# Performance work log

Hardware: AMD Instinct MI355X
Metric: run time of the kernel (lower is better)

The kernel has to match this reference:

```python
import jax, jax.numpy as jnp
import numpy as np


def setup_inputs() -> dict:
    key = jax.random.key(0)
    k1, k2, k3, k4, k5 = jax.random.split(key, 5)
    B, C, H, W = 4, 256, 64, 64
    INTER = 128
    # NOTE: original inits out.weight to zeros (residual identity at init);
    # we use small random weights so the reference exercises the full math.
    s = 0.02
    return {
        "x": jax.random.normal(k1, (B, C, H, W), dtype=jnp.float32),
        "w_theta": jax.random.normal(k2, (INTER, C), dtype=jnp.float32) * s,
        "w_phi": jax.random.normal(k3, (INTER, C), dtype=jnp.float32) * s,
        "w_g": jax.random.normal(k4, (INTER, C), dtype=jnp.float32) * s,
        "w_out": jax.random.normal(k5, (C, INTER), dtype=jnp.float32) * s,
    }


def reference(x, w_theta, w_phi, w_g, w_out):
    B, C, H, W = x.shape
    N = H * W
    xf = x.reshape(B, C, N)                      # [B, C, N]
    theta = jnp.einsum("ic,bcn->bni", w_theta, xf)  # [B, N, inter]
    phi = jnp.einsum("ic,bcn->bin", w_phi, xf)      # [B, inter, N]
    g = jnp.einsum("ic,bcn->bni", w_g, xf)          # [B, N, inter]
    attn = jax.nn.softmax(jnp.einsum("bni,bim->bnm", theta, phi), axis=-1)  # [B, N, N]
    y = jnp.einsum("bnm,bmi->bin", attn, g)         # [B, inter, N]
    out = jnp.einsum("ci,bin->bcn", w_out, y)       # [B, C, N]
    return x + out.reshape(B, C, H, W)
```

## Files before the change

kernel.cpp:

```cpp
#include <hip/hip_runtime.h>
#include <hip/hip_bf16.h>
#include <cstdint>

#define BATCH 4
#define CDIM 256
#define NTOK 4096
#define IDIM 128
#define NSP 8

typedef __attribute__((ext_vector_type(4))) float f32x4;
typedef __attribute__((ext_vector_type(16))) float f32x16;
typedef __attribute__((ext_vector_type(8))) short short8;

static __device__ __forceinline__ unsigned cvt_pk(float lo, float hi) {
  unsigned r;
  asm("v_cvt_pk_bf16_f32 %0, %1, %2" : "=v"(r) : "v"(lo), "v"(hi));
  return r;
}
static __device__ __forceinline__ float bf2f(unsigned short u) {
  union { unsigned u; float f; } v;
  v.u = (unsigned)u << 16;
  return v.f;
}
static __device__ __forceinline__ float exp2_f(float x) {
#if __has_builtin(__builtin_amdgcn_exp2f)
  return __builtin_amdgcn_exp2f(x);
#else
  return exp2f(x);
#endif
}
static __device__ __forceinline__ unsigned pk_fp8x4(float a, float b, float c, float d) {
  unsigned r = 0;
#if __has_builtin(__builtin_amdgcn_cvt_pk_fp8_f32)
  r = __builtin_amdgcn_cvt_pk_fp8_f32(a, b, r, false);
  r = __builtin_amdgcn_cvt_pk_fp8_f32(c, d, r, true);
#else
  asm("v_cvt_pk_fp8_f32 %0, %1, %2" : "+v"(r) : "v"(a), "v"(b));
  asm("v_cvt_pk_fp8_f32 %0, %1, %2 op_sel:[0,0,1]" : "+v"(r) : "v"(c), "v"(d));
#endif
  return r;
}

__global__ __launch_bounds__(256) void cast_w_kernel(
    const float* __restrict__ wt, const float* __restrict__ wp,
    const float* __restrict__ wg, const float* __restrict__ wo,
    unsigned short* __restrict__ Wb)
{
  int id = blockIdx.x * 256 + threadIdx.x;
  if (id < 24576) {
    int pidx = id >> 13;
    int rem = id & 8191;
    int i = rem >> 6, c4 = (rem & 63) * 4;
    const float* src = pidx == 0 ? wt : pidx == 1 ? wp : wg;
    float4 v = *(const float4*)&src[i * 256 + c4];
    float s = (pidx == 0) ? 1.4426950408889634f : 1.0f;
    uint2 u = make_uint2(cvt_pk(v.x * s, v.y * s), cvt_pk(v.z * s, v.w * s));
    *(uint2*)&Wb[(((size_t)pidx * 32 + (c4 >> 3)) * 128 + i) * 8 + (c4 & 7)] = u;
  } else {
    int rem = id - 24576;
    int c = rem >> 5, i4 = (rem & 31) * 4;
    float4 v = *(const float4*)&wo[c * 128 + i4];
    uint2 u = make_uint2(cvt_pk(v.x, v.y), cvt_pk(v.z, v.w));
    *(uint2*)&Wb[98304 + (((size_t)(i4 >> 3) * 256 + c) * 8) + (i4 & 7)] = u;
  }
}

__global__ __launch_bounds__(768) void qkv_kernel(
    const float* __restrict__ x, const unsigned short* __restrict__ Wb,
    unsigned char* __restrict__ Qf, unsigned char* __restrict__ Kf,
    unsigned short* __restrict__ Vf)
{
  __shared__ __align__(16) unsigned short xt[64 * 256];
  __shared__ __align__(16) unsigned short sc[8][16 * 128];

  const int b = blockIdx.y;
  const int n0 = blockIdx.x * 64;
  const int t = threadIdx.x;
  const float* xb = x + (size_t)b * CDIM * NTOK;

  for (int it = 0; it < 3; ++it) {
    int u = it * 768 + t;
    if (u < 2048) {
      int c0 = (u >> 4) * 2;
      int n4 = (u & 15) * 4;
      float4 va = *(const float4*)&xb[(size_t)c0 * NTOK + n0 + n4];
      float4 vb = *(const float4*)&xb[(size_t)(c0 + 1) * NTOK + n0 + n4];
      const float* pa = (const float*)&va;
      const float* pb = (const float*)&vb;
#pragma unroll
      for (int j = 0; j < 4; ++j) {
        int n = n4 + j;
        unsigned pk = cvt_pk(pa[j], pb[j]);
        *(unsigned*)((char*)xt + n * 512 + ((c0 * 2) ^ ((n & 15) << 4))) = pk;
      }
    }
  }
  __syncthreads();

  const int lane = t & 63;
  const int wv = __builtin_amdgcn_readfirstlane(t >> 6);
  const int nsub = wv & 3, proj = wv >> 2;
  const int cl = lane & 15, g = lane >> 4;

  f32x4 acc[8];
#pragma unroll
  for (int i = 0; i < 8; ++i) acc[i] = (f32x4){0.f, 0.f, 0.f, 0.f};

  const int nrow = nsub * 16 + cl;
  const int swz = (nrow & 15) << 4;
#pragma unroll
  for (int kc = 0; kc < 8; ++kc) {
    int cb = kc * 32 + g * 8;
    short8 af = *(const short8*)((const char*)xt + nrow * 512 + ((cb * 2) ^ swz));
#pragma unroll
    for (int is = 0; is < 8; ++is) {
      short8 bf = *(const short8*)&Wb[(((size_t)proj * 32 + kc * 4 + g) * 128 +
                                       is * 16 + cl) * 8];
      acc[is] = __builtin_amdgcn_mfma_f32_16x16x32_bf16(af, bf, acc[is], 0, 0, 0);
    }
  }

  if (proj < 2) {
    unsigned short* scw = sc[wv];
#pragma unroll
    for (int is = 0; is < 8; ++is)
#pragma unroll
      for (int r = 0; r < 4; ++r) {
        int nl = g * 4 + r;
        int i2 = (is * 16 + cl) * 2;
        *(unsigned short*)((char*)scw + nl * 256 + (i2 ^ ((nl & 15) << 4))) =
            (unsigned short)cvt_pk(acc[is][r], 0.f);
      }
    unsigned char* dstF = (proj == 0 ? Qf : Kf) + (size_t)b * (NTOK * IDIM);
    const int r = lane & 15;
    const int n = n0 + nsub * 16 + r;
    const size_t ntbase = (size_t)(n >> 5) * 4096;
#pragma unroll
    for (int u = 0; u < 4; ++u) {
      int c = (lane >> 4) + 4 * u;
      short8 v8 = *(const short8*)((const char*)scw + r * 256 +
                                   ((c * 16) ^ ((r & 15) << 4)));
      float f[8];
#pragma unroll
      for (int e = 0; e < 8; ++e) f[e] = bf2f((unsigned short)v8[e]);
      uint2 w = make_uint2(pk_fp8x4(f[0], f[1], f[2], f[3]),
                           pk_fp8x4(f[4], f[5], f[6], f[7]));
      size_t off = ntbase + (size_t)(c >> 1) * 512 +
                   (size_t)((n & 31) + 32 * (c & 1)) * 8;
      *(uint2*)(dstF + off) = w;
    }
  } else {
    unsigned short* dstV = Vf + (size_t)b * (IDIM * NTOK) +
                           (size_t)((n0 >> 4) + nsub) * 2048;
#pragma unroll
    for (int is = 0; is < 8; ++is) {
      int itv = is >> 1;
      int l2 = (is & 1) * 16 + cl + 32 * (g >> 1);
      uint2 u = make_uint2(cvt_pk(acc[is][0], acc[is][1]),
                           cvt_pk(acc[is][2], acc[is][3]));
      *(uint2*)&dstV[itv * 512 + l2 * 8 + (g & 1) * 4] = u;
    }
  }
}

__global__ __launch_bounds__(64) void attn_kernel(
    const unsigned char* __restrict__ Qf, const unsigned char* __restrict__ Kf,
    const unsigned short* __restrict__ Vf, unsigned short* __restrict__ Op,
    float* __restrict__ Lp)
{
  const int bid = blockIdx.x;
  const int b = (bid >> 1) & 3;
  const int ms = (bid >> 3) & 7;
  const int nb = (bid >> 6) * 2 + (bid & 1);
  const int lane = threadIdx.x & 63;
  const int n0 = nb * 32;
  const int c32 = lane & 31, hl = lane >> 5;

  const unsigned char* Kfb = Kf + (size_t)b * (NTOK * IDIM);
  const unsigned short* Vfb = Vf + (size_t)b * (IDIM * NTOK);

  const unsigned char* Qp = Qf + (size_t)b * (NTOK * IDIM) +
                            (size_t)nb * 4096 + lane * 8;
  long q8[8];
#pragma unroll
  for (int kc = 0; kc < 8; ++kc) q8[kc] = *(const long*)(Qp + kc * 512);

  f32x16 o[4];
#pragma unroll
  for (int it = 0; it < 4; ++it)
#pragma unroll
    for (int e = 0; e < 16; ++e) o[it][e] = 0.f;
  float Ll = 0.f;

  const int t0 = ms * 16;
  for (int tt = 0; tt < 16; ++tt) {
    const unsigned char* Kt = Kfb + (size_t)(t0 + tt) * 4096;
    const unsigned short* Vt = Vfb + (size_t)(t0 + tt) * 4096;

    long ka[8];
#pragma unroll
    for (int kc = 0; kc < 8; ++kc) ka[kc] = *(const long*)(Kt + kc * 512 + lane * 8);
    short8 vf[8];
#pragma unroll
    for (int it = 0; it < 4; ++it)
#pragma unroll
      for (int kt = 0; kt < 2; ++kt)
        vf[it * 2 + kt] = *(const short8*)&Vt[kt * 2048 + it * 512 + lane * 8];

    f32x16 sa, sb;
#pragma unroll
    for (int e = 0; e < 16; ++e) { sa[e] = 0.f; sb[e] = 0.f; }
    __builtin_amdgcn_s_setprio(1);
#pragma unroll
    for (int kc = 0; kc < 4; ++kc) {
      sa = __builtin_amdgcn_mfma_f32_32x32x16_fp8_fp8(ka[kc], q8[kc], sa, 0, 0, 0);
      sb = __builtin_amdgcn_mfma_f32_32x32x16_fp8_fp8(ka[kc + 4], q8[kc + 4], sb, 0, 0, 0);
    }
    __builtin_amdgcn_s_setprio(0);

    float pr[16];
#pragma unroll
    for (int e = 0; e < 16; ++e) pr[e] = exp2_f(sa[e] + sb[e]);
    float sv[8];
#pragma unroll
    for (int j = 0; j < 8; ++j) sv[j] = pr[j] + pr[j + 8];
#pragma unroll
    for (int j = 0; j < 4; ++j) sv[j] += sv[j + 4];
    Ll += (sv[0] + sv[1]) + (sv[2] + sv[3]);

    short8 pf[2];
#pragma unroll
    for (int kt = 0; kt < 2; ++kt) {
      unsigned a0 = cvt_pk(pr[kt * 8 + 0], pr[kt * 8 + 1]);
      unsigned a1 = cvt_pk(pr[kt * 8 + 2], pr[kt * 8 + 3]);
      unsigned a2 = cvt_pk(pr[kt * 8 + 4], pr[kt * 8 + 5]);
      unsigned a3 = cvt_pk(pr[kt * 8 + 6], pr[kt * 8 + 7]);
      asm volatile("v_permlane32_swap_b32 %0, %1" : "+v"(a0), "+v"(a2));
      asm volatile("v_permlane32_swap_b32 %0, %1" : "+v"(a1), "+v"(a3));
      union { unsigned u[4]; short8 s; } w;
      w.u[0] = a0; w.u[1] = a1; w.u[2] = a2; w.u[3] = a3;
      pf[kt] = w.s;
    }

    __builtin_amdgcn_s_setprio(1);
#pragma unroll
    for (int it = 0; it < 4; ++it) {
#pragma unroll
      for (int kt = 0; kt < 2; ++kt)
        o[it] = __builtin_amdgcn_mfma_f32_32x32x16_bf16(vf[it * 2 + kt], pf[kt],
                                                        o[it], 0, 0, 0);
    }
    __builtin_amdgcn_s_setprio(0);
  }

  {
    const int sb2 = ms * 4 + b;
    unsigned short* Ob = Op + (size_t)sb2 * (16 * NTOK * 8);
#pragma unroll
    for (int it = 0; it < 4; ++it)
#pragma unroll
      for (int g2 = 0; g2 < 4; ++g2) {
        uint2 u2 = make_uint2(cvt_pk(o[it][4 * g2 + 0], o[it][4 * g2 + 1]),
                              cvt_pk(o[it][4 * g2 + 2], o[it][4 * g2 + 3]));
        *(uint2*)&Ob[((size_t)(it * 4 + g2) * NTOK + n0 + c32) * 8 + 4 * hl] = u2;
      }
    Ll += __shfl_xor(Ll, 32);
    if (hl == 0) Lp[(size_t)sb2 * NTOK + n0 + c32] = Ll;
  }
}

__global__ __launch_bounds__(256) void out_kernel(
    const float* __restrict__ x, const unsigned short* __restrict__ Wb,
    const unsigned short* __restrict__ Op, const float* __restrict__ Lp,
    float* __restrict__ out)
{
  const int b = blockIdx.y;
  const int n0 = blockIdx.x * 32;
  const int t = threadIdx.x;
  const int lane = t & 63;
  const int wv = __builtin_amdgcn_readfirstlane(t >> 6);
  const int cl = lane & 15, g = lane >> 4;

  float rinv[2];
#pragma unroll
  for (int nsb = 0; nsb < 2; ++nsb) {
    int n = n0 + nsb * 16 + cl;
    float Lx = 0.f;
#pragma unroll
    for (int s = 0; s < NSP; ++s) Lx += Lp[(size_t)(s * 4 + b) * NTOK + n];
    rinv[nsb] = 1.f / Lx;
  }

  f32x4 acc[4][2];
#pragma unroll
  for (int cs = 0; cs < 4; ++cs)
#pragma unroll
    for (int nsb = 0; nsb < 2; ++nsb) acc[cs][nsb] = (f32x4){0.f, 0.f, 0.f, 0.f};

#pragma unroll
  for (int kc = 0; kc < 4; ++kc) {
    short8 bf[2];
#pragma unroll
    for (int nsb = 0; nsb < 2; ++nsb) {
      int n = n0 + nsb * 16 + cl;
      size_t base = ((size_t)(kc * 4 + g) * NTOK + n) * 8;
      float a[8];
#pragma unroll
      for (int e = 0; e < 8; ++e) a[e] = 0.f;
#pragma unroll
      for (int s = 0; s < NSP; ++s) {
        const short8 f = *(const short8*)&Op[(size_t)(s * 4 + b) * (16 * NTOK * 8) + base];
#pragma unroll
        for (int e = 0; e < 8; ++e) a[e] += bf2f((unsigned short)f[e]);
      }
      union { unsigned u[4]; short8 s8; } r;
#pragma unroll
      for (int jp = 0; jp < 4; ++jp)
        r.u[jp] = cvt_pk(a[2 * jp] * rinv[nsb], a[2 * jp + 1] * rinv[nsb]);
      bf[nsb] = r.s8;
    }
#pragma unroll
    for (int cs = 0; cs < 4; ++cs) {
      short8 af = *(const short8*)&Wb[98304 +
          (((size_t)(kc * 4 + g)) * 256 + wv * 64 + cs * 16 + cl) * 8];
#pragma unroll
      for (int nsb = 0; nsb < 2; ++nsb)
        acc[cs][nsb] = __builtin_amdgcn_mfma_f32_16x16x32_bf16(af, bf[nsb], acc[cs][nsb], 0, 0, 0);
    }
  }

  const float* xb = x + (size_t)b * CDIM * NTOK;
  float* ob = out + (size_t)b * CDIM * NTOK;
#pragma unroll
  for (int cs = 0; cs < 4; ++cs)
#pragma unroll
    for (int nsb = 0; nsb < 2; ++nsb)
#pragma unroll
      for (int r = 0; r < 4; ++r) {
        int c = wv * 64 + cs * 16 + g * 4 + r;
        int n = n0 + nsb * 16 + cl;
        ob[(size_t)c * NTOK + n] = xb[(size_t)c * NTOK + n] + acc[cs][nsb][r];
      }
}

extern "C" void kernel_launch(void* const* d_in, const int* in_sizes, int n_in,
                              void* d_out, int out_size, void* d_ws, size_t ws_size,
                              hipStream_t stream) {
  const float* x  = (const float*)d_in[0];
  const float* wt = (const float*)d_in[1];
  const float* wp = (const float*)d_in[2];
  const float* wg = (const float*)d_in[3];
  const float* wo = (const float*)d_in[4];
  float* outp = (float*)d_out;

  char* ws = (char*)d_ws;
  unsigned short* Wb = (unsigned short*)(ws);
  unsigned char* Qf  = (unsigned char*)(ws + (size_t)1 * (1 << 20));
  unsigned char* Kf  = (unsigned char*)(ws + (size_t)3 * (1 << 20));
  unsigned short* Vfd = (unsigned short*)(ws + (size_t)5 * (1 << 20));
  unsigned short* Opd = (unsigned short*)(ws + (size_t)9 * (1 << 20));
  float* Lpd = (float*)(ws + (size_t)41 * (1 << 20));

  cast_w_kernel<<<128, 256, 0, stream>>>(wt, wp, wg, wo, Wb);
  qkv_kernel<<<dim3(64, BATCH), 768, 0, stream>>>(x, Wb, Qf, Kf, Vfd);
  attn_kernel<<<4096, 64, 0, stream>>>(Qf, Kf, Vfd, Opd, Lpd);
  out_kernel<<<dim3(128, BATCH), 256, 0, stream>>>(x, Wb, Opd, Lpd, outp);
}
```

Baseline: 78.46 us.

## Process two query tiles per wave to reuse K/V fragment loads

```diff
diff --git a/kernel.cpp b/kernel.cpp
--- a/kernel.cpp
+++ b/kernel.cpp
@@ -163,7 +163,7 @@
   }
 }
 
-__global__ __launch_bounds__(64) void attn_kernel(
+__global__ __launch_bounds__(128, 2) void attn_kernel(
     const unsigned char* __restrict__ Qf, const unsigned char* __restrict__ Kf,
     const unsigned short* __restrict__ Vf, unsigned short* __restrict__ Op,
     float* __restrict__ Lp)
@@ -171,26 +171,31 @@
   const int bid = blockIdx.x;
   const int b = (bid >> 1) & 3;
   const int ms = (bid >> 3) & 7;
-  const int nb = (bid >> 6) * 2 + (bid & 1);
+  const int nb128 = (bid >> 6) * 2 + (bid & 1);
+  const int wv = threadIdx.x >> 6;
   const int lane = threadIdx.x & 63;
-  const int n0 = nb * 32;
+  const int nb32 = nb128 * 4 + wv * 2;
+  const int n0 = nb32 * 32;
   const int c32 = lane & 31, hl = lane >> 5;
 
   const unsigned char* Kfb = Kf + (size_t)b * (NTOK * IDIM);
   const unsigned short* Vfb = Vf + (size_t)b * (IDIM * NTOK);
 
   const unsigned char* Qp = Qf + (size_t)b * (NTOK * IDIM) +
-                            (size_t)nb * 4096 + lane * 8;
-  long q8[8];
-#pragma unroll
-  for (int kc = 0; kc < 8; ++kc) q8[kc] = *(const long*)(Qp + kc * 512);
-
-  f32x16 o[4];
+                            (size_t)nb32 * 4096 + lane * 8;
+  long q8a[8], q8b[8];
+#pragma unroll
+  for (int kc = 0; kc < 8; ++kc) {
+    q8a[kc] = *(const long*)(Qp + kc * 512);
+    q8b[kc] = *(const long*)(Qp + 4096 + kc * 512);
+  }
+
+  f32x16 o0[4], o1[4];
 #pragma unroll
   for (int it = 0; it < 4; ++it)
 #pragma unroll
-    for (int e = 0; e < 16; ++e) o[it][e] = 0.f;
-  float Ll = 0.f;
+    for (int e = 0; e < 16; ++e) { o0[it][e] = 0.f; o1[it][e] = 0.f; }
+  float Ll0 = 0.f, Ll1 = 0.f;
 
   const int t0 = ms * 16;
   for (int tt = 0; tt < 16; ++tt) {
@@ -207,48 +212,84 @@
       for (int kt = 0; kt < 2; ++kt)
         vf[it * 2 + kt] = *(const short8*)&Vt[kt * 2048 + it * 512 + lane * 8];
 
-    f32x16 sa, sb;
-#pragma unroll
-    for (int e = 0; e < 16; ++e) { sa[e] = 0.f; sb[e] = 0.f; }
+    short8 pf0[2], pf1[2];
+    {
+      f32x16 sa, sb;
+#pragma unroll
+      for (int e = 0; e < 16; ++e) { sa[e] = 0.f; sb[e] = 0.f; }
+      __builtin_amdgcn_s_setprio(1);
+#pragma unroll
+      for (int kc = 0; kc < 4; ++kc) {
+        sa = __builtin_amdgcn_mfma_f32_32x32x16_fp8_fp8(ka[kc], q8a[kc], sa, 0, 0, 0);
+        sb = __builtin_amdgcn_mfma_f32_32x32x16_fp8_fp8(ka[kc + 4], q8a[kc + 4], sb, 0, 0, 0);
+      }
+      __builtin_amdgcn_s_setprio(0);
+      float pr[16];
+#pragma unroll
+      for (int e = 0; e < 16; ++e) pr[e] = exp2_f(sa[e] + sb[e]);
+      float sv[8];
+#pragma unroll
+      for (int j = 0; j < 8; ++j) sv[j] = pr[j] + pr[j + 8];
+#pragma unroll
+      for (int j = 0; j < 4; ++j) sv[j] += sv[j + 4];
+      Ll0 += (sv[0] + sv[1]) + (sv[2] + sv[3]);
+#pragma unroll
+      for (int kt = 0; kt < 2; ++kt) {
+        unsigned a0 = cvt_pk(pr[kt * 8 + 0], pr[kt * 8 + 1]);
+        unsigned a1 = cvt_pk(pr[kt * 8 + 2], pr[kt * 8 + 3]);
+        unsigned a2 = cvt_pk(pr[kt * 8 + 4], pr[kt * 8 + 5]);
+        unsigned a3 = cvt_pk(pr[kt * 8 + 6], pr[kt * 8 + 7]);
+        asm volatile("v_permlane32_swap_b32 %0, %1" : "+v"(a0), "+v"(a2));
+        asm volatile("v_permlane32_swap_b32 %0, %1" : "+v"(a1), "+v"(a3));
+        union { unsigned u[4]; short8 s; } w;
+        w.u[0] = a0; w.u[1] = a1; w.u[2] = a2; w.u[3] = a3;
+        pf0[kt] = w.s;
+      }
+    }
+    {
+      f32x16 sa, sb;
+#pragma unroll
+      for (int e = 0; e < 16; ++e) { sa[e] = 0.f; sb[e] = 0.f; }
+      __builtin_amdgcn_s_setprio(1);
+#pragma unroll
+      for (int kc = 0; kc < 4; ++kc) {
+        sa = __builtin_amdgcn_mfma_f32_32x32x16_fp8_fp8(ka[kc], q8b[kc], sa, 0, 0, 0);
+        sb = __builtin_amdgcn_mfma_f32_32x32x16_fp8_fp8(ka[kc + 4], q8b[kc + 4], sb, 0, 0, 0);
+      }
+      __builtin_amdgcn_s_setprio(0);
+      float pr[16];
+#pragma unroll
+      for (int e = 0; e < 16; ++e) pr[e] = exp2_f(sa[e] + sb[e]);
+      float sv[8];
+#pragma unroll
+      for (int j = 0; j < 8; ++j) sv[j] = pr[j] + pr[j + 8];
+#pragma unroll
+      for (int j = 0; j < 4; ++j) sv[j] += sv[j + 4];
+      Ll1 += (sv[0] + sv[1]) + (sv[2] + sv[3]);
+#pragma unroll
+      for (int kt = 0; kt < 2; ++kt) {
+        unsigned a0 = cvt_pk(pr[kt * 8 + 0], pr[kt * 8 + 1]);
+        unsigned a1 = cvt_pk(pr[kt * 8 + 2], pr[kt * 8 + 3]);
+        unsigned a2 = cvt_pk(pr[kt * 8 + 4], pr[kt * 8 + 5]);
+        unsigned a3 = cvt_pk(pr[kt * 8 + 6], pr[kt * 8 + 7]);
+        asm volatile("v_permlane32_swap_b32 %0, %1" : "+v"(a0), "+v"(a2));
+        asm volatile("v_permlane32_swap_b32 %0, %1" : "+v"(a1), "+v"(a3));
+        union { unsigned u[4]; short8 s; } w;
+        w.u[0] = a0; w.u[1] = a1; w.u[2] = a2; w.u[3] = a3;
+        pf1[kt] = w.s;
+      }
+    }
+
     __builtin_amdgcn_s_setprio(1);
 #pragma unroll
-    for (int kc = 0; kc < 4; ++kc) {
-      sa = __builtin_amdgcn_mfma_f32_32x32x16_fp8_fp8(ka[kc], q8[kc], sa, 0, 0, 0);
-      sb = __builtin_amdgcn_mfma_f32_32x32x16_fp8_fp8(ka[kc + 4], q8[kc + 4], sb, 0, 0, 0);
-    }
-    __builtin_amdgcn_s_setprio(0);
-
-    float pr[16];
-#pragma unroll
-    for (int e = 0; e < 16; ++e) pr[e] = exp2_f(sa[e] + sb[e]);
-    float sv[8];
-#pragma unroll
-    for (int j = 0; j < 8; ++j) sv[j] = pr[j] + pr[j + 8];
-#pragma unroll
-    for (int j = 0; j < 4; ++j) sv[j] += sv[j + 4];
-    Ll += (sv[0] + sv[1]) + (sv[2] + sv[3]);
-
-    short8 pf[2];
-#pragma unroll
-    for (int kt = 0; kt < 2; ++kt) {
-      unsigned a0 = cvt_pk(pr[kt * 8 + 0], pr[kt * 8 + 1]);
-      unsigned a1 = cvt_pk(pr[kt * 8 + 2], pr[kt * 8 + 3]);
-      unsigned a2 = cvt_pk(pr[kt * 8 + 4], pr[kt * 8 + 5]);
-      unsigned a3 = cvt_pk(pr[kt * 8 + 6], pr[kt * 8 + 7]);
-      asm volatile("v_permlane32_swap_b32 %0, %1" : "+v"(a0), "+v"(a2));
-      asm volatile("v_permlane32_swap_b32 %0, %1" : "+v"(a1), "+v"(a3));
-      union { unsigned u[4]; short8 s; } w;
-      w.u[0] = a0; w.u[1] = a1; w.u[2] = a2; w.u[3] = a3;
-      pf[kt] = w.s;
-    }
-
-    __builtin_amdgcn_s_setprio(1);
-#pragma unroll
     for (int it = 0; it < 4; ++it) {
 #pragma unroll
-      for (int kt = 0; kt < 2; ++kt)
-        o[it] = __builtin_amdgcn_mfma_f32_32x32x16_bf16(vf[it * 2 + kt], pf[kt],
-                                                        o[it], 0, 0, 0);
+      for (int kt = 0; kt < 2; ++kt) {
+        o0[it] = __builtin_amdgcn_mfma_f32_32x32x16_bf16(vf[it * 2 + kt], pf0[kt],
+                                                         o0[it], 0, 0, 0);
+        o1[it] = __builtin_amdgcn_mfma_f32_32x32x16_bf16(vf[it * 2 + kt], pf1[kt],
+                                                         o1[it], 0, 0, 0);
+      }
     }
     __builtin_amdgcn_s_setprio(0);
   }
@@ -260,12 +301,19 @@
     for (int it = 0; it < 4; ++it)
 #pragma unroll
       for (int g2 = 0; g2 < 4; ++g2) {
-        uint2 u2 = make_uint2(cvt_pk(o[it][4 * g2 + 0], o[it][4 * g2 + 1]),
-                              cvt_pk(o[it][4 * g2 + 2], o[it][4 * g2 + 3]));
-        *(uint2*)&Ob[((size_t)(it * 4 + g2) * NTOK + n0 + c32) * 8 + 4 * hl] = u2;
-      }
-    Ll += __shfl_xor(Ll, 32);
-    if (hl == 0) Lp[(size_t)sb2 * NTOK + n0 + c32] = Ll;
+        uint2 ua = make_uint2(cvt_pk(o0[it][4 * g2 + 0], o0[it][4 * g2 + 1]),
+                              cvt_pk(o0[it][4 * g2 + 2], o0[it][4 * g2 + 3]));
+        *(uint2*)&Ob[((size_t)(it * 4 + g2) * NTOK + n0 + c32) * 8 + 4 * hl] = ua;
+        uint2 ub = make_uint2(cvt_pk(o1[it][4 * g2 + 0], o1[it][4 * g2 + 1]),
+                              cvt_pk(o1[it][4 * g2 + 2], o1[it][4 * g2 + 3]));
+        *(uint2*)&Ob[((size_t)(it * 4 + g2) * NTOK + n0 + 32 + c32) * 8 + 4 * hl] = ub;
+      }
+    Ll0 += __shfl_xor(Ll0, 32);
+    Ll1 += __shfl_xor(Ll1, 32);
+    if (hl == 0) {
+      Lp[(size_t)sb2 * NTOK + n0 + c32] = Ll0;
+      Lp[(size_t)sb2 * NTOK + n0 + 32 + c32] = Ll1;
+    }
   }
 }
 
@@ -363,6 +411,6 @@
 
   cast_w_kernel<<<128, 256, 0, stream>>>(wt, wp, wg, wo, Wb);
   qkv_kernel<<<dim3(64, BATCH), 768, 0, stream>>>(x, Wb, Qf, Kf, Vfd);
-  attn_kernel<<<4096, 64, 0, stream>>>(Qf, Kf, Vfd, Opd, Lpd);
+  attn_kernel<<<1024, 128, 0, stream>>>(Qf, Kf, Vfd, Opd, Lpd);
   out_kernel<<<dim3(128, BATCH), 256, 0, stream>>>(x, Wb, Opd, Lpd, outp);
 }
```

New measurement: 99.79 us. +27.2%, slower.

## Share K/V tiles across four waves via async LDS double buffering in attention

Applied to the files above, without the earlier changes.

```diff
diff --git a/kernel.cpp b/kernel.cpp
--- a/kernel.cpp
+++ b/kernel.cpp
@@ -39,6 +39,11 @@
   asm("v_cvt_pk_fp8_f32 %0, %1, %2 op_sel:[0,0,1]" : "+v"(r) : "v"(c), "v"(d));
 #endif
   return r;
+}
+static __device__ __forceinline__ void gl16(const void* g, void* l) {
+  __builtin_amdgcn_global_load_lds(
+      (const __attribute__((address_space(1))) void*)g,
+      (__attribute__((address_space(3))) void*)l, 16, 0, 0);
 }
 
 __global__ __launch_bounds__(256) void cast_w_kernel(
@@ -163,24 +168,30 @@
   }
 }
 
-__global__ __launch_bounds__(64) void attn_kernel(
+__global__ __launch_bounds__(256, 2) void attn_kernel(
     const unsigned char* __restrict__ Qf, const unsigned char* __restrict__ Kf,
     const unsigned short* __restrict__ Vf, unsigned short* __restrict__ Op,
     float* __restrict__ Lp)
 {
+  __shared__ __align__(16) unsigned char kls[2][4096];
+  __shared__ __align__(16) unsigned short vls[2][4096];
+
   const int bid = blockIdx.x;
   const int b = (bid >> 1) & 3;
   const int ms = (bid >> 3) & 7;
-  const int nb = (bid >> 6) * 2 + (bid & 1);
-  const int lane = threadIdx.x & 63;
-  const int n0 = nb * 32;
+  const int nslab = (bid >> 6) * 2 + (bid & 1);
+  const int t = threadIdx.x;
+  const int lane = t & 63;
+  const int wv = t >> 6;
+  const int nb32 = nslab * 4 + wv;
+  const int n0 = nb32 * 32;
   const int c32 = lane & 31, hl = lane >> 5;
 
   const unsigned char* Kfb = Kf + (size_t)b * (NTOK * IDIM);
   const unsigned short* Vfb = Vf + (size_t)b * (IDIM * NTOK);
 
   const unsigned char* Qp = Qf + (size_t)b * (NTOK * IDIM) +
-                            (size_t)nb * 4096 + lane * 8;
+                            (size_t)nb32 * 4096 + lane * 8;
   long q8[8];
 #pragma unroll
   for (int kc = 0; kc < 8; ++kc) q8[kc] = *(const long*)(Qp + kc * 512);
@@ -192,20 +203,26 @@
     for (int e = 0; e < 16; ++e) o[it][e] = 0.f;
   float Ll = 0.f;
 
+#define STAGE_K(cb, mt_)                                                      \
+  gl16(Kfb + (size_t)(mt_)*4096 + t * 16, (char*)kls[cb] + t * 16);
+#define STAGE_V(cb, mt_)                                                      \
+  {                                                                           \
+    const char* Vit = (const char*)(Vfb + (size_t)(mt_)*4096);                \
+    gl16(Vit + t * 16, (char*)vls[cb] + t * 16);                              \
+    gl16(Vit + t * 16 + 4096, (char*)vls[cb] + t * 16 + 4096);                \
+  }
+
   const int t0 = ms * 16;
+  asm volatile("s_waitcnt vmcnt(0)" ::: "memory");
+  STAGE_K(0, t0)
+  STAGE_V(0, t0)
+  STAGE_K(1, t0 + 1)
+
   for (int tt = 0; tt < 16; ++tt) {
-    const unsigned char* Kt = Kfb + (size_t)(t0 + tt) * 4096;
-    const unsigned short* Vt = Vfb + (size_t)(t0 + tt) * 4096;
-
-    long ka[8];
-#pragma unroll
-    for (int kc = 0; kc < 8; ++kc) ka[kc] = *(const long*)(Kt + kc * 512 + lane * 8);
-    short8 vf[8];
-#pragma unroll
-    for (int it = 0; it < 4; ++it)
-#pragma unroll
-      for (int kt = 0; kt < 2; ++kt)
-        vf[it * 2 + kt] = *(const short8*)&Vt[kt * 2048 + it * 512 + lane * 8];
+    asm volatile("s_waitcnt vmcnt(3)\n\ts_barrier" ::: "memory");
+
+    const char* kbuf = (const char*)kls[tt & 1];
+    const char* vbuf = (const char*)vls[tt & 1];
 
     f32x16 sa, sb;
 #pragma unroll
@@ -213,8 +230,10 @@
     __builtin_amdgcn_s_setprio(1);
 #pragma unroll
     for (int kc = 0; kc < 4; ++kc) {
-      sa = __builtin_amdgcn_mfma_f32_32x32x16_fp8_fp8(ka[kc], q8[kc], sa, 0, 0, 0);
-      sb = __builtin_amdgcn_mfma_f32_32x32x16_fp8_fp8(ka[kc + 4], q8[kc + 4], sb, 0, 0, 0);
+      long ka = *(const long*)(kbuf + kc * 512 + lane * 8);
+      long kb2 = *(const long*)(kbuf + (kc + 4) * 512 + lane * 8);
+      sa = __builtin_amdgcn_mfma_f32_32x32x16_fp8_fp8(ka, q8[kc], sa, 0, 0, 0);
+      sb = __builtin_amdgcn_mfma_f32_32x32x16_fp8_fp8(kb2, q8[kc + 4], sb, 0, 0, 0);
     }
     __builtin_amdgcn_s_setprio(0);
 
@@ -242,16 +261,27 @@
       pf[kt] = w.s;
     }
 
+    asm volatile("s_waitcnt vmcnt(1)\n\ts_barrier" ::: "memory");
+    {
+      int mv = t0 + (tt >= 15 ? 15 : tt + 1);
+      int mk = t0 + (tt >= 14 ? 15 : tt + 2);
+      STAGE_V((tt + 1) & 1, mv)
+      STAGE_K(tt & 1, mk)
+    }
+
     __builtin_amdgcn_s_setprio(1);
 #pragma unroll
     for (int it = 0; it < 4; ++it) {
 #pragma unroll
-      for (int kt = 0; kt < 2; ++kt)
-        o[it] = __builtin_amdgcn_mfma_f32_32x32x16_bf16(vf[it * 2 + kt], pf[kt],
-                                                        o[it], 0, 0, 0);
+      for (int kt = 0; kt < 2; ++kt) {
+        short8 vf2 = *(const short8*)(vbuf + kt * 4096 + it * 1024 + lane * 16);
+        o[it] = __builtin_amdgcn_mfma_f32_32x32x16_bf16(vf2, pf[kt], o[it], 0, 0, 0);
+      }
     }
     __builtin_amdgcn_s_setprio(0);
   }
+#undef STAGE_K
+#undef STAGE_V
 
   {
     const int sb2 = ms * 4 + b;
@@ -363,6 +393,6 @@
 
   cast_w_kernel<<<128, 256, 0, stream>>>(wt, wp, wg, wo, Wb);
   qkv_kernel<<<dim3(64, BATCH), 768, 0, stream>>>(x, Wb, Qf, Kf, Vfd);
-  attn_kernel<<<4096, 64, 0, stream>>>(Qf, Kf, Vfd, Opd, Lpd);
+  attn_kernel<<<1024, 256, 0, stream>>>(Qf, Kf, Vfd, Opd, Lpd);
   out_kernel<<<dim3(128, BATCH), 256, 0, stream>>>(x, Wb, Opd, Lpd, outp);
 }
```

Measured after the change: 70.86 us. 9.7% less time.
